# Kernel tuning notes

Measured on AMD Instinct MI355X. Metric: run time of the kernel, lower is better.

## Reference

```python
import jax, jax.numpy as jnp
import numpy as np

B, N, F, E, D, H, L = 4, 2048, 2, 16, 32, 4, 2
GRAPH_LAYERS = 3
FLOW_ITERS = 10
COST_C = 1.0        # quadratic cost: c*x^2, inv_derivative(y) = y/(2c)
BIG_NUMBER = 1e7


def setup_inputs():
    key = jax.random.key(0)
    ks = jax.random.split(key, 20)
    node_features = jax.random.normal(ks[0], (B, N, F), jnp.float32)
    node_embeddings = jax.random.normal(ks[1], (B, N, E), jnp.float32)
    demands = jax.random.normal(ks[2], (B, N, 1), jnp.float32)
    demands = demands - demands.mean(axis=1, keepdims=True)  # flow conservation
    adj = (jax.random.uniform(ks[3], (B, N, N)) < 0.01).astype(jnp.float32)
    adj = adj * (1.0 - jnp.eye(N, dtype=jnp.float32))
    eye = jnp.broadcast_to(jnp.eye(N, dtype=jnp.float32), (B, N, N))
    neighborhoods = jnp.stack([eye, adj], axis=1)  # [B,L,N,N] hop-0 and hop-1
    def g(k, shape):
        return jax.random.normal(k, shape, jnp.float32) * 0.1
    params = {
        'We1': g(ks[4], (E + F, D)), 'be1': jnp.zeros((D,), jnp.float32),
        'We2': g(ks[5], (D, D)), 'be2': jnp.zeros((D,), jnp.float32),
        'w_attn': g(ks[6], (H, D)),
        'Wo': g(ks[7], (D, D)), 'bo': jnp.zeros((D,), jnp.float32),
        'Wz': g(ks[8], (D, D)), 'Uz': g(ks[9], (D, D)), 'bz': jnp.zeros((D,), jnp.float32),
        'Wr': g(ks[10], (D, D)), 'Ur': g(ks[11], (D, D)), 'br': jnp.zeros((D,), jnp.float32),
        'Wh': g(ks[12], (D, D)), 'Uh': g(ks[13], (D, D)), 'bh': jnp.zeros((D,), jnp.float32),
        'Wd1': g(ks[14], (D, D)), 'bd1': jnp.zeros((D,), jnp.float32),
        'Wd2': g(ks[15], (D, 1)), 'bd2': jnp.zeros((1,), jnp.float32),
        'Wv1': g(ks[16], (D, D)), 'bv1': jnp.zeros((D,), jnp.float32),
        'Wv2': g(ks[17], (D, 1)), 'bv2': jnp.zeros((1,), jnp.float32),
    }
    return {'node_features': node_features, 'node_embeddings': node_embeddings,
            'demands': demands, 'adj': adj, 'neighborhoods': neighborhoods, **params}


def _forward(node_features, node_embeddings, demands, adj, neighborhoods,
             We1, be1, We2, be2, w_attn, Wo, bo,
             Wz, Uz, bz, Wr, Ur, br, Wh, Uh, bh,
             Wd1, bd1, Wd2, bd2, Wv1, bv1, Wv2, bv2):
    # --- node encoder MLP (tanh, activate_final=True) ---
    x = jnp.concatenate([node_embeddings, node_features], axis=-1)   # [B,N,E+F]
    enc = jnp.tanh(jnp.tanh(x @ We1 + be1) @ We2 + be2)               # [B,N,D]
    # row-normalized neighborhood operators (degree-normalized aggregation)
    Mnorm = neighborhoods / (jnp.sum(neighborhoods, axis=-1, keepdims=True) + 1.0)
    # --- graph_layers x (attention neighborhood + GRU state update) ---
    for _ in range(GRAPH_LAYERS):
        agg = jnp.einsum('blnm,bmd->blnd', Mnorm, enc)                # [B,L,N,D]
        scores = jnp.einsum('blnd,hd->bhnl', jnp.tanh(agg), w_attn)   # [B,H,N,L]
        alpha = jax.nn.softmax(scores, axis=-1)
        ctx = jnp.einsum('bhnl,blnd->bnd', alpha, agg) / H            # mean over heads
        nbr = jnp.tanh(ctx @ Wo + bo)                                 # [B,N,D]
        z = jax.nn.sigmoid(nbr @ Wz + enc @ Uz + bz)
        r = jax.nn.sigmoid(nbr @ Wr + enc @ Ur + br)
        h = jnp.tanh(nbr @ Wh + (r * enc) @ Uh + bh)
        enc = z * enc + (1.0 - z) * h
    # --- primal: edge weights, masked softmax, proportional flow solver ---
    pred = (enc @ Wd1 + bd1) @ Wd2 + bd2                              # [B,N,1]
    pw = pred * jnp.transpose(pred, (0, 2, 1))                        # [B,N,N]
    weights = -BIG_NUMBER * (1.0 - adj) + pw
    fwp = jax.nn.softmax(weights, axis=-1)                            # rows sum to 1
    flow0 = fwp * jax.nn.relu(-demands)

    def step(flow, _):
        inflow = jnp.sum(flow, axis=1)[..., None]                     # [B,N,1]
        return fwp * jax.nn.relu(inflow - demands), None

    flow, _ = jax.lax.scan(step, flow0, None, length=FLOW_ITERS)
    flow_cost = jnp.sum(COST_C * flow * flow, axis=(1, 2))            # [B]
    # --- dual: dual variables, dual flows via inverse cost derivative ---
    dual = (enc @ Wv1 + bv1) @ Wv2 + bv2                              # [B,N,1]
    dd = dual - jnp.transpose(dual, (0, 2, 1))                        # [B,N,N]
    df = adj * jax.nn.relu(dd / (2.0 * COST_C))
    dual_cost = jnp.sum(COST_C * df * df - dd * df, axis=(1, 2)) \
        - jnp.sum(dual * demands, axis=(1, 2))                        # [B]
    return flow_cost - dual_cost                                      # primal-dual gap loss, [B]


def reference(node_features, node_embeddings, demands, adj, neighborhoods,
              We1, be1, We2, be2, w_attn, Wo, bo,
              Wz, Uz, bz, Wr, Ur, br, Wh, Uh, bh,
              Wd1, bd1, Wd2, bd2, Wv1, bv1, Wv2, bv2):
    return _forward(node_features, node_embeddings, demands, adj, neighborhoods,
                    We1, be1, We2, be2, w_attn, Wo, bo,
                    Wz, Uz, bz, Wr, Ur, br, Wh, Uh, bh,
                    Wd1, bd1, Wd2, bd2, Wv1, bv1, Wv2, bv2)
```

## Files before the change

kernel.cpp:

```cpp
#include <hip/hip_runtime.h>

#define NN 2048
#define NB 4
#define BN (NB * NN)
#define MAXD 96

__global__ __launch_bounds__(256) void k_front(
    const float* __restrict__ feat, const float* __restrict__ emb,
    const float* __restrict__ We1, const float* __restrict__ be1,
    const float* __restrict__ We2, const float* __restrict__ be2,
    float* __restrict__ enc_out,
    const float* __restrict__ adj, int* __restrict__ deg, int* __restrict__ cols,
    int* __restrict__ tdeg)
{
    int tid = threadIdx.x;
    if (blockIdx.x < 1024) {
        __shared__ float sW1[18 * 32], sb1[32], sW2[32 * 32], sb2[32];
        for (int i = tid; i < 18 * 32; i += 256) sW1[i] = We1[i];
        for (int i = tid; i < 32 * 32; i += 256) sW2[i] = We2[i];
        if (tid < 32) { sb1[tid] = be1[tid]; sb2[tid] = be2[tid]; }
        __syncthreads();
        int group = tid >> 5, j = tid & 31;
        int node = blockIdx.x * 8 + group;
        float x;
        if (j < 16)      x = emb[node * 16 + j];
        else if (j < 18) x = feat[node * 2 + (j - 16)];
        else             x = 0.f;
        float acc = sb1[j];
#pragma unroll
        for (int k = 0; k < 18; k++)
            acc += __shfl(x, k, 32) * sW1[k * 32 + j];
        float h = tanhf(acc);
        float acc2 = sb2[j];
#pragma unroll
        for (int k = 0; k < 32; k++)
            acc2 += __shfl(h, k, 32) * sW2[k * 32 + j];
        enc_out[node * 32 + j] = tanhf(acc2);
    } else {
        int wave = tid >> 6, lane = tid & 63;
        int row = (blockIdx.x - 1024) * 4 + wave;
        const float4* p = (const float4*)(adj + (size_t)row * NN);
        int cnt = 0;
        int base = row * MAXD;
#pragma unroll
        for (int it = 0; it < 8; it++) {
            float4 v = p[it * 64 + lane];
            float va[4] = { v.x, v.y, v.z, v.w };
#pragma unroll
            for (int c = 0; c < 4; c++) {
                unsigned long long m = __ballot(va[c] != 0.f);
                if (va[c] != 0.f) {
                    int pos = cnt + __popcll(m & ((1ull << lane) - 1ull));
                    if (pos < MAXD) cols[base + pos] = it * 256 + lane * 4 + c;
                }
                cnt += __popcll(m);
            }
        }
        if (lane == 0) {
            deg[row] = cnt < MAXD ? cnt : MAXD;
            tdeg[row] = 0;
        }
    }
}

__global__ __launch_bounds__(256) void k_layer(
    const float* __restrict__ enc_in, float* __restrict__ enc_out,
    const int* __restrict__ deg, const int* __restrict__ cols,
    const float* __restrict__ w_attn,
    const float* __restrict__ Wo, const float* __restrict__ bo,
    const float* __restrict__ Wz, const float* __restrict__ Uz, const float* __restrict__ bz,
    const float* __restrict__ Wr, const float* __restrict__ Ur, const float* __restrict__ br,
    const float* __restrict__ Wh, const float* __restrict__ Uh, const float* __restrict__ bh)
{
    __shared__ float sWo[1024], sWz[1024], sUz[1024], sWr[1024], sUr[1024], sWh[1024], sUh[1024];
    __shared__ float sbo[32], sbz[32], sbr[32], sbh[32], sAttn[128];
    int tid = threadIdx.x;
    for (int i = tid; i < 1024; i += 256) {
        sWo[i] = Wo[i]; sWz[i] = Wz[i]; sUz[i] = Uz[i];
        sWr[i] = Wr[i]; sUr[i] = Ur[i]; sWh[i] = Wh[i]; sUh[i] = Uh[i];
    }
    if (tid < 32) { sbo[tid] = bo[tid]; sbz[tid] = bz[tid]; sbr[tid] = br[tid]; sbh[tid] = bh[tid]; }
    if (tid < 128) sAttn[tid] = w_attn[tid];
    __syncthreads();
    int group = tid >> 5, j = tid & 31;
    int node = blockIdx.x * 8 + group;
    int b = node >> 11;
    const float* encB = enc_in + (size_t)(b * NN) * 32;
    float e = enc_in[node * 32 + j];
    float agg0 = 0.5f * e;
    int d = deg[node];
    const int* cp = cols + node * MAXD;
    float a1 = 0.f;
    for (int i = 0; i < d; i++) {
        int m = cp[i];
        a1 += encB[m * 32 + j];
    }
    a1 *= 1.0f / (float)(d + 1);
    float t0 = tanhf(agg0), t1 = tanhf(a1);
    float sc[8];
#pragma unroll
    for (int h2 = 0; h2 < 4; h2++) { sc[h2] = sAttn[h2 * 32 + j] * t0; sc[4 + h2] = sAttn[h2 * 32 + j] * t1; }
#pragma unroll
    for (int off = 16; off >= 1; off >>= 1)
#pragma unroll
        for (int q = 0; q < 8; q++) sc[q] += __shfl_xor(sc[q], off, 32);
    float c0 = 0.f, c1 = 0.f;
#pragma unroll
    for (int h2 = 0; h2 < 4; h2++) {
        float a = sc[h2], bsc = sc[4 + h2];
        float mx = fmaxf(a, bsc);
        float e0 = expf(a - mx), e1 = expf(bsc - mx);
        float inv = 1.0f / (e0 + e1);
        c0 += e0 * inv; c1 += e1 * inv;
    }
    c0 *= 0.25f; c1 *= 0.25f;
    float ctx = c0 * agg0 + c1 * a1;
    float acc = sbo[j];
#pragma unroll
    for (int k = 0; k < 32; k++) acc += __shfl(ctx, k, 32) * sWo[k * 32 + j];
    float nbr = tanhf(acc);
    float az = sbz[j], ar = sbr[j], ah = sbh[j];
#pragma unroll
    for (int k = 0; k < 32; k++) {
        float nb = __shfl(nbr, k, 32);
        float en = __shfl(e, k, 32);
        az += nb * sWz[k * 32 + j] + en * sUz[k * 32 + j];
        ar += nb * sWr[k * 32 + j] + en * sUr[k * 32 + j];
        ah += nb * sWh[k * 32 + j];
    }
    float z = 1.0f / (1.0f + expf(-az));
    float r = 1.0f / (1.0f + expf(-ar));
    float re = r * e;
#pragma unroll
    for (int k = 0; k < 32; k++) ah += __shfl(re, k, 32) * sUh[k * 32 + j];
    float hc = tanhf(ah);
    enc_out[node * 32 + j] = z * e + (1.0f - z) * hc;
}

__global__ __launch_bounds__(256) void k_heads(
    const float* __restrict__ enc,
    const float* __restrict__ Wd1, const float* __restrict__ bd1,
    const float* __restrict__ Wd2, const float* __restrict__ bd2,
    const float* __restrict__ Wv1, const float* __restrict__ bv1,
    const float* __restrict__ Wv2, const float* __restrict__ bv2,
    float* __restrict__ pred, float* __restrict__ dual)
{
    __shared__ float sWd1[1024], sWv1[1024], sbd1[32], sbv1[32], sWd2[32], sWv2[32];
    int tid = threadIdx.x;
    for (int i = tid; i < 1024; i += 256) { sWd1[i] = Wd1[i]; sWv1[i] = Wv1[i]; }
    if (tid < 32) { sbd1[tid] = bd1[tid]; sbv1[tid] = bv1[tid]; sWd2[tid] = Wd2[tid]; sWv2[tid] = Wv2[tid]; }
    __syncthreads();
    int group = tid >> 5, j = tid & 31;
    int node = blockIdx.x * 8 + group;
    float e = enc[node * 32 + j];
    float ad = sbd1[j], av = sbv1[j];
#pragma unroll
    for (int k = 0; k < 32; k++) {
        float en = __shfl(e, k, 32);
        ad += en * sWd1[k * 32 + j];
        av += en * sWv1[k * 32 + j];
    }
    float pd = ad * sWd2[j];
    float dv = av * sWv2[j];
#pragma unroll
    for (int off = 16; off >= 1; off >>= 1) {
        pd += __shfl_xor(pd, off, 32);
        dv += __shfl_xor(dv, off, 32);
    }
    if (j == 0) {
        pred[node] = pd + bd2[0];
        dual[node] = dv + bv2[0];
    }
}

__global__ __launch_bounds__(256) void k_edge_scatter(
    const int* __restrict__ deg, const int* __restrict__ cols,
    const float* __restrict__ pred, const float* __restrict__ dual,
    int* __restrict__ tdeg, int* __restrict__ tcols, float* __restrict__ tvals,
    float* __restrict__ rowsq, float* __restrict__ rowdual)
{
    int wave = threadIdx.x >> 6, lane = threadIdx.x & 63;
    int row = blockIdx.x * 4 + wave;
    int b = row >> 11;
    int rloc = row & (NN - 1);
    const float* predB = pred + b * NN;
    const float* dualB = dual + b * NN;
    int d = deg[row];
    int base = row * MAXD;
    float pn = pred[row];
    float dn = dual[row];
    float mx = -1e30f;
    for (int i = lane; i < d; i += 64) {
        int c = cols[base + i];
        mx = fmaxf(mx, pn * predB[c]);
    }
#pragma unroll
    for (int off = 32; off >= 1; off >>= 1) mx = fmaxf(mx, __shfl_xor(mx, off));
    float den = 0.f, du = 0.f;
    for (int i = lane; i < d; i += 64) {
        int c = cols[base + i];
        den += expf(pn * predB[c] - mx);
        float dd = dn - dualB[c];
        if (dd > 0.f) du -= 0.25f * dd * dd;
    }
#pragma unroll
    for (int off = 32; off >= 1; off >>= 1) { den += __shfl_xor(den, off); du += __shfl_xor(du, off); }
    float invden = 1.0f / den;
    float rs = 0.f;
    for (int i = lane; i < d; i += 64) {
        int c = cols[base + i];
        float f = expf(pn * predB[c] - mx) * invden;
        rs += f * f;
        int pos = atomicAdd(&tdeg[b * NN + c], 1);
        if (pos < MAXD) {
            size_t idx = (size_t)(b * MAXD + pos) * NN + c;
            tcols[idx] = rloc;
            tvals[idx] = f;
        }
    }
#pragma unroll
    for (int off = 32; off >= 1; off >>= 1) rs += __shfl_xor(rs, off);
    if (lane == 0) { rowsq[row] = rs; rowdual[row] = du; }
}

__global__ __launch_bounds__(1024) void k_flow_batch(
    const int* __restrict__ tdeg, const int* __restrict__ tcols,
    const float* __restrict__ tvals, const float* __restrict__ demands,
    const float* __restrict__ rowsq, const float* __restrict__ rowdual,
    const float* __restrict__ dual, float* __restrict__ out)
{
    __shared__ float sdem[NN], sA[NN], sBuf[NN];
    __shared__ float red[3][16];
    int tid = threadIdx.x;
    int b = blockIdx.x;
    const float* demB = demands + b * NN;
    for (int n = tid; n < NN; n += 1024) {
        float dm = demB[n];
        sdem[n] = dm;
        sA[n] = fmaxf(-dm, 0.f);
    }
    __syncthreads();
    int n0 = tid, n1 = tid + 1024;
    int d0 = tdeg[b * NN + n0];
    int d1 = tdeg[b * NN + n1];
    const int* tc = tcols + (size_t)b * MAXD * NN;
    const float* tv = tvals + (size_t)b * MAXD * NN;
#pragma unroll 1
    for (int it = 0; it < 5; it++) {
        {
            float a0 = 0.f, a1 = 0.f;
            for (int i = 0; i < d0; i++) a0 += tv[i * NN + n0] * sA[tc[i * NN + n0]];
            for (int i = 0; i < d1; i++) a1 += tv[i * NN + n1] * sA[tc[i * NN + n1]];
            sBuf[n0] = fmaxf(a0 - sdem[n0], 0.f);
            sBuf[n1] = fmaxf(a1 - sdem[n1], 0.f);
        }
        __syncthreads();
        {
            float a0 = 0.f, a1 = 0.f;
            for (int i = 0; i < d0; i++) a0 += tv[i * NN + n0] * sBuf[tc[i * NN + n0]];
            for (int i = 0; i < d1; i++) a1 += tv[i * NN + n1] * sBuf[tc[i * NN + n1]];
            sA[n0] = fmaxf(a0 - sdem[n0], 0.f);
            sA[n1] = fmaxf(a1 - sdem[n1], 0.f);
        }
        __syncthreads();
    }
    float fc = 0.f, ds = 0.f, dq = 0.f;
    for (int n = tid; n < NN; n += 1024) {
        int row = b * NN + n;
        float sv = sA[n];
        fc += rowsq[row] * sv * sv;
        ds += rowdual[row];
        dq += dual[row] * sdem[n];
    }
#pragma unroll
    for (int off = 32; off >= 1; off >>= 1) {
        fc += __shfl_xor(fc, off);
        ds += __shfl_xor(ds, off);
        dq += __shfl_xor(dq, off);
    }
    int wv = tid >> 6;
    if ((tid & 63) == 0) { red[0][wv] = fc; red[1][wv] = ds; red[2][wv] = dq; }
    __syncthreads();
    if (tid == 0) {
        float a = 0.f, s1 = 0.f, s2 = 0.f;
        for (int w = 0; w < 16; w++) { a += red[0][w]; s1 += red[1][w]; s2 += red[2][w]; }
        out[b] = a - s1 + s2;
    }
}

extern "C" void kernel_launch(void* const* d_in, const int* in_sizes, int n_in,
                              void* d_out, int out_size, void* d_ws, size_t ws_size,
                              hipStream_t stream) {
    const float* feat = (const float*)d_in[0];
    const float* emb  = (const float*)d_in[1];
    const float* dem  = (const float*)d_in[2];
    const float* adj  = (const float*)d_in[3];
    const float* We1 = (const float*)d_in[5];
    const float* be1 = (const float*)d_in[6];
    const float* We2 = (const float*)d_in[7];
    const float* be2 = (const float*)d_in[8];
    const float* w_attn = (const float*)d_in[9];
    const float* Wo = (const float*)d_in[10];
    const float* bo = (const float*)d_in[11];
    const float* Wz = (const float*)d_in[12];
    const float* Uz = (const float*)d_in[13];
    const float* bz = (const float*)d_in[14];
    const float* Wr = (const float*)d_in[15];
    const float* Ur = (const float*)d_in[16];
    const float* br = (const float*)d_in[17];
    const float* Wh = (const float*)d_in[18];
    const float* Uh = (const float*)d_in[19];
    const float* bh = (const float*)d_in[20];
    const float* Wd1 = (const float*)d_in[21];
    const float* bd1 = (const float*)d_in[22];
    const float* Wd2 = (const float*)d_in[23];
    const float* bd2 = (const float*)d_in[24];
    const float* Wv1 = (const float*)d_in[25];
    const float* bv1 = (const float*)d_in[26];
    const float* Wv2 = (const float*)d_in[27];
    const float* bv2 = (const float*)d_in[28];
    float* out = (float*)d_out;

    float* w = (float*)d_ws;
    float* enc0 = w;            w += (size_t)BN * 32;
    float* enc1 = w;            w += (size_t)BN * 32;
    int*   degp = (int*)w;      w += BN;
    int*   colp = (int*)w;      w += (size_t)BN * MAXD;
    float* pred = w;            w += BN;
    float* dual = w;            w += BN;
    float* rowsq = w;           w += BN;
    float* rowdual = w;         w += BN;
    int*   tdeg = (int*)w;      w += BN;
    int*   tcol = (int*)w;      w += (size_t)BN * MAXD;
    float* tval = w;            w += (size_t)BN * MAXD;

    k_front<<<3072, 256, 0, stream>>>(feat, emb, We1, be1, We2, be2, enc0,
                                      adj, degp, colp, tdeg);
    k_layer<<<BN / 8, 256, 0, stream>>>(enc0, enc1, degp, colp, w_attn,
                                        Wo, bo, Wz, Uz, bz, Wr, Ur, br, Wh, Uh, bh);
    k_layer<<<BN / 8, 256, 0, stream>>>(enc1, enc0, degp, colp, w_attn,
                                        Wo, bo, Wz, Uz, bz, Wr, Ur, br, Wh, Uh, bh);
    k_layer<<<BN / 8, 256, 0, stream>>>(enc0, enc1, degp, colp, w_attn,
                                        Wo, bo, Wz, Uz, bz, Wr, Ur, br, Wh, Uh, bh);
    k_heads<<<BN / 8, 256, 0, stream>>>(enc1, Wd1, bd1, Wd2, bd2, Wv1, bv1, Wv2, bv2,
                                        pred, dual);
    k_edge_scatter<<<BN / 4, 256, 0, stream>>>(degp, colp, pred, dual,
                                               tdeg, tcol, tval, rowsq, rowdual);
    k_flow_batch<<<NB, 1024, 0, stream>>>(tdeg, tcol, tval, dem,
                                          rowsq, rowdual, dual, out);
}
```

Before: 461.5 us.

## Pack transposed edges per node as float2 and shuffle-broadcast neighbor indices

The transposed edge storage changes from separate column-major index and value arrays to a per-node contiguous array of (value, column) float2 pairs, which the flow kernel reads as float4 with two accumulators. The layer kernel loads neighbor indices once per lane and broadcasts them via warp shuffles, with dual accumulators. The aim is to cut index-load latency and serial dependency chains. The packed per-node layout makes adjacent threads read strided addresses, so it gives up the coalescing of the previous layout.

```diff
diff --git a/kernel.cpp b/kernel.cpp
--- a/kernel.cpp
+++ b/kernel.cpp
@@ -90,12 +90,24 @@
     float agg0 = 0.5f * e;
     int d = deg[node];
     const int* cp = cols + node * MAXD;
-    float a1 = 0.f;
-    for (int i = 0; i < d; i++) {
-        int m = cp[i];
+    int iA = cp[j];
+    int iB = cp[j + 32];
+    float a1 = 0.f, a1b = 0.f;
+    int dmin = d < 32 ? d : 32;
+#pragma unroll 4
+    for (int i = 0; i < dmin - 1; i += 2) {
+        int m0 = __shfl(iA, i, 32);
+        int m1 = __shfl(iA, i + 1, 32);
+        a1  += encB[m0 * 32 + j];
+        a1b += encB[m1 * 32 + j];
+    }
+    if (dmin & 1) { int m = __shfl(iA, dmin - 1, 32); a1 += encB[m * 32 + j]; }
+#pragma unroll 2
+    for (int i = 32; i < d; i++) {
+        int m = __shfl(iB, i - 32, 32);
         a1 += encB[m * 32 + j];
     }
-    a1 *= 1.0f / (float)(d + 1);
+    a1 = (a1 + a1b) * (1.0f / (float)(d + 1));
     float t0 = tanhf(agg0), t1 = tanhf(a1);
     float sc[8];
 #pragma unroll
@@ -176,7 +188,7 @@
 __global__ __launch_bounds__(256) void k_edge_scatter(
     const int* __restrict__ deg, const int* __restrict__ cols,
     const float* __restrict__ pred, const float* __restrict__ dual,
-    int* __restrict__ tdeg, int* __restrict__ tcols, float* __restrict__ tvals,
+    int* __restrict__ tdeg, float2* __restrict__ pk,
     float* __restrict__ rowsq, float* __restrict__ rowdual)
 {
     int wave = threadIdx.x >> 6, lane = threadIdx.x & 63;
@@ -213,9 +225,7 @@
         rs += f * f;
         int pos = atomicAdd(&tdeg[b * NN + c], 1);
         if (pos < MAXD) {
-            size_t idx = (size_t)(b * MAXD + pos) * NN + c;
-            tcols[idx] = rloc;
-            tvals[idx] = f;
+            pk[((size_t)(b * NN) + c) * MAXD + pos] = make_float2(f, __int_as_float(rloc));
         }
     }
 #pragma unroll
@@ -223,9 +233,31 @@
     if (lane == 0) { rowsq[row] = rs; rowdual[row] = du; }
 }
 
+#define FLOW_GATHER(EPTR, PAIRS, REM, DTOT, SRC, ACC_A, ACC_B)                     \
+    {                                                                              \
+        int i_ = 0;                                                                \
+        for (; i_ + 1 < (PAIRS); i_ += 2) {                                        \
+            float4 qa_ = (EPTR)[i_];                                               \
+            float4 qb_ = (EPTR)[i_ + 1];                                           \
+            ACC_A += qa_.x * SRC[__float_as_int(qa_.y)];                           \
+            ACC_B += qa_.z * SRC[__float_as_int(qa_.w)];                           \
+            ACC_A += qb_.x * SRC[__float_as_int(qb_.y)];                           \
+            ACC_B += qb_.z * SRC[__float_as_int(qb_.w)];                           \
+        }                                                                          \
+        if (i_ < (PAIRS)) {                                                        \
+            float4 q_ = (EPTR)[i_];                                                \
+            ACC_A += q_.x * SRC[__float_as_int(q_.y)];                             \
+            ACC_B += q_.z * SRC[__float_as_int(q_.w)];                             \
+        }                                                                          \
+        if (REM) {                                                                 \
+            float2 q_ = ((const float2*)(EPTR))[(DTOT) - 1];                       \
+            ACC_A += q_.x * SRC[__float_as_int(q_.y)];                             \
+        }                                                                          \
+    }
+
 __global__ __launch_bounds__(1024) void k_flow_batch(
-    const int* __restrict__ tdeg, const int* __restrict__ tcols,
-    const float* __restrict__ tvals, const float* __restrict__ demands,
+    const int* __restrict__ tdeg, const float2* __restrict__ pk,
+    const float* __restrict__ demands,
     const float* __restrict__ rowsq, const float* __restrict__ rowdual,
     const float* __restrict__ dual, float* __restrict__ out)
 {
@@ -243,24 +275,27 @@
     int n0 = tid, n1 = tid + 1024;
     int d0 = tdeg[b * NN + n0];
     int d1 = tdeg[b * NN + n1];
-    const int* tc = tcols + (size_t)b * MAXD * NN;
-    const float* tv = tvals + (size_t)b * MAXD * NN;
+    const float4* e0 = (const float4*)(pk + ((size_t)(b * NN) + n0) * MAXD);
+    const float4* e1 = (const float4*)(pk + ((size_t)(b * NN) + n1) * MAXD);
+    int p0 = d0 >> 1, r0 = d0 & 1;
+    int p1 = d1 >> 1, r1 = d1 & 1;
+    float dm0 = sdem[n0], dm1 = sdem[n1];
 #pragma unroll 1
     for (int it = 0; it < 5; it++) {
         {
-            float a0 = 0.f, a1 = 0.f;
-            for (int i = 0; i < d0; i++) a0 += tv[i * NN + n0] * sA[tc[i * NN + n0]];
-            for (int i = 0; i < d1; i++) a1 += tv[i * NN + n1] * sA[tc[i * NN + n1]];
-            sBuf[n0] = fmaxf(a0 - sdem[n0], 0.f);
-            sBuf[n1] = fmaxf(a1 - sdem[n1], 0.f);
+            float a0 = 0.f, a0b = 0.f, a1 = 0.f, a1b = 0.f;
+            FLOW_GATHER(e0, p0, r0, d0, sA, a0, a0b);
+            FLOW_GATHER(e1, p1, r1, d1, sA, a1, a1b);
+            sBuf[n0] = fmaxf(a0 + a0b - dm0, 0.f);
+            sBuf[n1] = fmaxf(a1 + a1b - dm1, 0.f);
         }
         __syncthreads();
         {
-            float a0 = 0.f, a1 = 0.f;
-            for (int i = 0; i < d0; i++) a0 += tv[i * NN + n0] * sBuf[tc[i * NN + n0]];
-            for (int i = 0; i < d1; i++) a1 += tv[i * NN + n1] * sBuf[tc[i * NN + n1]];
-            sA[n0] = fmaxf(a0 - sdem[n0], 0.f);
-            sA[n1] = fmaxf(a1 - sdem[n1], 0.f);
+            float a0 = 0.f, a0b = 0.f, a1 = 0.f, a1b = 0.f;
+            FLOW_GATHER(e0, p0, r0, d0, sBuf, a0, a0b);
+            FLOW_GATHER(e1, p1, r1, d1, sBuf, a1, a1b);
+            sA[n0] = fmaxf(a0 + a0b - dm0, 0.f);
+            sA[n1] = fmaxf(a1 + a1b - dm1, 0.f);
         }
         __syncthreads();
     }
@@ -331,8 +366,7 @@
     float* rowsq = w;           w += BN;
     float* rowdual = w;         w += BN;
     int*   tdeg = (int*)w;      w += BN;
-    int*   tcol = (int*)w;      w += (size_t)BN * MAXD;
-    float* tval = w;            w += (size_t)BN * MAXD;
+    float2* pk = (float2*)w;    w += (size_t)BN * MAXD * 2;
 
     k_front<<<3072, 256, 0, stream>>>(feat, emb, We1, be1, We2, be2, enc0,
                                       adj, degp, colp, tdeg);
@@ -345,7 +379,7 @@
     k_heads<<<BN / 8, 256, 0, stream>>>(enc1, Wd1, bd1, Wd2, bd2, Wv1, bv1, Wv2, bv2,
                                         pred, dual);
     k_edge_scatter<<<BN / 4, 256, 0, stream>>>(degp, colp, pred, dual,
-                                               tdeg, tcol, tval, rowsq, rowdual);
-    k_flow_batch<<<NB, 1024, 0, stream>>>(tdeg, tcol, tval, dem,
+                                               tdeg, pk, rowsq, rowdual);
+    k_flow_batch<<<NB, 1024, 0, stream>>>(tdeg, pk, dem,
                                           rowsq, rowdual, dual, out);
 }
```

Measured after the change: 476.3 us. 1.03x slower.

## Fuse heads into last GNN layer, enlarge layer blocks, shuffle-broadcast neighbor indices

Applied to the files above, without the earlier changes.

The last graph layer now also computes the decoder and dual heads, which removes one kernel launch and the round trip of the final encoding through global memory. Layer blocks grow from 256 to 1024 threads (32 nodes per block), so the shared-memory weight staging is spread over more nodes. Neighbor indices are loaded once per lane and broadcast with shuffles, and the gather loop uses two accumulators to overlap loads. The larger blocks raise per-block shared memory and may limit occupancy, and the dual accumulators change floating-point summation order.

```diff
diff --git a/kernel.cpp b/kernel.cpp
--- a/kernel.cpp
+++ b/kernel.cpp
@@ -63,7 +63,75 @@
     }
 }
 
-__global__ __launch_bounds__(256) void k_layer(
+__device__ __forceinline__ float layer_body(
+    int node, int j, int d, const int* __restrict__ cp,
+    const float* __restrict__ encB, float e,
+    const float* sAttn, const float* sWo, const float* sbo,
+    const float* sWz, const float* sUz, const float* sbz,
+    const float* sWr, const float* sUr, const float* sbr,
+    const float* sWh, const float* sUh, const float* sbh)
+{
+    float agg0 = 0.5f * e;
+    int iA = cp[j];
+    int iB = cp[j + 32];
+    float a1 = 0.f, a1b = 0.f;
+    int dmin = d < 32 ? d : 32;
+#pragma unroll 4
+    for (int i = 0; i < dmin - 1; i += 2) {
+        int m0 = __shfl(iA, i, 32);
+        int m1 = __shfl(iA, i + 1, 32);
+        a1  += encB[m0 * 32 + j];
+        a1b += encB[m1 * 32 + j];
+    }
+    if (dmin & 1) { int m = __shfl(iA, dmin - 1, 32); a1 += encB[m * 32 + j]; }
+#pragma unroll 2
+    for (int i = 32; i < d; i++) {
+        int m = __shfl(iB, i - 32, 32);
+        a1 += encB[m * 32 + j];
+    }
+    a1 = (a1 + a1b) * (1.0f / (float)(d + 1));
+    float t0 = tanhf(agg0), t1 = tanhf(a1);
+    float sc[8];
+#pragma unroll
+    for (int h2 = 0; h2 < 4; h2++) { sc[h2] = sAttn[h2 * 32 + j] * t0; sc[4 + h2] = sAttn[h2 * 32 + j] * t1; }
+#pragma unroll
+    for (int off = 16; off >= 1; off >>= 1)
+#pragma unroll
+        for (int q = 0; q < 8; q++) sc[q] += __shfl_xor(sc[q], off, 32);
+    float c0 = 0.f, c1 = 0.f;
+#pragma unroll
+    for (int h2 = 0; h2 < 4; h2++) {
+        float a = sc[h2], bsc = sc[4 + h2];
+        float mx = fmaxf(a, bsc);
+        float e0 = expf(a - mx), e1 = expf(bsc - mx);
+        float inv = 1.0f / (e0 + e1);
+        c0 += e0 * inv; c1 += e1 * inv;
+    }
+    c0 *= 0.25f; c1 *= 0.25f;
+    float ctx = c0 * agg0 + c1 * a1;
+    float acc = sbo[j];
+#pragma unroll
+    for (int k = 0; k < 32; k++) acc += __shfl(ctx, k, 32) * sWo[k * 32 + j];
+    float nbr = tanhf(acc);
+    float az = sbz[j], ar = sbr[j], ah = sbh[j];
+#pragma unroll
+    for (int k = 0; k < 32; k++) {
+        float nb = __shfl(nbr, k, 32);
+        float en = __shfl(e, k, 32);
+        az += nb * sWz[k * 32 + j] + en * sUz[k * 32 + j];
+        ar += nb * sWr[k * 32 + j] + en * sUr[k * 32 + j];
+        ah += nb * sWh[k * 32 + j];
+    }
+    float z = 1.0f / (1.0f + expf(-az));
+    float r = 1.0f / (1.0f + expf(-ar));
+    float re = r * e;
+#pragma unroll
+    for (int k = 0; k < 32; k++) ah += __shfl(re, k, 32) * sUh[k * 32 + j];
+    float hc = tanhf(ah);
+    return z * e + (1.0f - z) * hc;
+}
+
+__global__ __launch_bounds__(1024) void k_layer(
     const float* __restrict__ enc_in, float* __restrict__ enc_out,
     const int* __restrict__ deg, const int* __restrict__ cols,
     const float* __restrict__ w_attn,
@@ -75,7 +143,8 @@
     __shared__ float sWo[1024], sWz[1024], sUz[1024], sWr[1024], sUr[1024], sWh[1024], sUh[1024];
     __shared__ float sbo[32], sbz[32], sbr[32], sbh[32], sAttn[128];
     int tid = threadIdx.x;
-    for (int i = tid; i < 1024; i += 256) {
+    {
+        int i = tid;
         sWo[i] = Wo[i]; sWz[i] = Wz[i]; sUz[i] = Uz[i];
         sWr[i] = Wr[i]; sUr[i] = Ur[i]; sWh[i] = Wh[i]; sUh[i] = Uh[i];
     }
@@ -83,80 +152,61 @@
     if (tid < 128) sAttn[tid] = w_attn[tid];
     __syncthreads();
     int group = tid >> 5, j = tid & 31;
-    int node = blockIdx.x * 8 + group;
+    int node = blockIdx.x * 32 + group;
     int b = node >> 11;
     const float* encB = enc_in + (size_t)(b * NN) * 32;
     float e = enc_in[node * 32 + j];
-    float agg0 = 0.5f * e;
     int d = deg[node];
     const int* cp = cols + node * MAXD;
-    float a1 = 0.f;
-    for (int i = 0; i < d; i++) {
-        int m = cp[i];
-        a1 += encB[m * 32 + j];
-    }
-    a1 *= 1.0f / (float)(d + 1);
-    float t0 = tanhf(agg0), t1 = tanhf(a1);
-    float sc[8];
-#pragma unroll
-    for (int h2 = 0; h2 < 4; h2++) { sc[h2] = sAttn[h2 * 32 + j] * t0; sc[4 + h2] = sAttn[h2 * 32 + j] * t1; }
-#pragma unroll
-    for (int off = 16; off >= 1; off >>= 1)
-#pragma unroll
-        for (int q = 0; q < 8; q++) sc[q] += __shfl_xor(sc[q], off, 32);
-    float c0 = 0.f, c1 = 0.f;
-#pragma unroll
-    for (int h2 = 0; h2 < 4; h2++) {
-        float a = sc[h2], bsc = sc[4 + h2];
-        float mx = fmaxf(a, bsc);
-        float e0 = expf(a - mx), e1 = expf(bsc - mx);
-        float inv = 1.0f / (e0 + e1);
-        c0 += e0 * inv; c1 += e1 * inv;
-    }
-    c0 *= 0.25f; c1 *= 0.25f;
-    float ctx = c0 * agg0 + c1 * a1;
-    float acc = sbo[j];
-#pragma unroll
-    for (int k = 0; k < 32; k++) acc += __shfl(ctx, k, 32) * sWo[k * 32 + j];
-    float nbr = tanhf(acc);
-    float az = sbz[j], ar = sbr[j], ah = sbh[j];
-#pragma unroll
-    for (int k = 0; k < 32; k++) {
-        float nb = __shfl(nbr, k, 32);
-        float en = __shfl(e, k, 32);
-        az += nb * sWz[k * 32 + j] + en * sUz[k * 32 + j];
-        ar += nb * sWr[k * 32 + j] + en * sUr[k * 32 + j];
-        ah += nb * sWh[k * 32 + j];
-    }
-    float z = 1.0f / (1.0f + expf(-az));
-    float r = 1.0f / (1.0f + expf(-ar));
-    float re = r * e;
-#pragma unroll
-    for (int k = 0; k < 32; k++) ah += __shfl(re, k, 32) * sUh[k * 32 + j];
-    float hc = tanhf(ah);
-    enc_out[node * 32 + j] = z * e + (1.0f - z) * hc;
-}
-
-__global__ __launch_bounds__(256) void k_heads(
-    const float* __restrict__ enc,
+    float eo = layer_body(node, j, d, cp, encB, e, sAttn, sWo, sbo,
+                          sWz, sUz, sbz, sWr, sUr, sbr, sWh, sUh, sbh);
+    enc_out[node * 32 + j] = eo;
+}
+
+__global__ __launch_bounds__(1024) void k_layer_last(
+    const float* __restrict__ enc_in,
+    const int* __restrict__ deg, const int* __restrict__ cols,
+    const float* __restrict__ w_attn,
+    const float* __restrict__ Wo, const float* __restrict__ bo,
+    const float* __restrict__ Wz, const float* __restrict__ Uz, const float* __restrict__ bz,
+    const float* __restrict__ Wr, const float* __restrict__ Ur, const float* __restrict__ br,
+    const float* __restrict__ Wh, const float* __restrict__ Uh, const float* __restrict__ bh,
     const float* __restrict__ Wd1, const float* __restrict__ bd1,
     const float* __restrict__ Wd2, const float* __restrict__ bd2,
     const float* __restrict__ Wv1, const float* __restrict__ bv1,
     const float* __restrict__ Wv2, const float* __restrict__ bv2,
     float* __restrict__ pred, float* __restrict__ dual)
 {
-    __shared__ float sWd1[1024], sWv1[1024], sbd1[32], sbv1[32], sWd2[32], sWv2[32];
+    __shared__ float sWo[1024], sWz[1024], sUz[1024], sWr[1024], sUr[1024], sWh[1024], sUh[1024];
+    __shared__ float sWd1[1024], sWv1[1024];
+    __shared__ float sbo[32], sbz[32], sbr[32], sbh[32], sAttn[128];
+    __shared__ float sbd1[32], sbv1[32], sWd2[32], sWv2[32];
     int tid = threadIdx.x;
-    for (int i = tid; i < 1024; i += 256) { sWd1[i] = Wd1[i]; sWv1[i] = Wv1[i]; }
-    if (tid < 32) { sbd1[tid] = bd1[tid]; sbv1[tid] = bv1[tid]; sWd2[tid] = Wd2[tid]; sWv2[tid] = Wv2[tid]; }
+    {
+        int i = tid;
+        sWo[i] = Wo[i]; sWz[i] = Wz[i]; sUz[i] = Uz[i];
+        sWr[i] = Wr[i]; sUr[i] = Ur[i]; sWh[i] = Wh[i]; sUh[i] = Uh[i];
+        sWd1[i] = Wd1[i]; sWv1[i] = Wv1[i];
+    }
+    if (tid < 32) {
+        sbo[tid] = bo[tid]; sbz[tid] = bz[tid]; sbr[tid] = br[tid]; sbh[tid] = bh[tid];
+        sbd1[tid] = bd1[tid]; sbv1[tid] = bv1[tid]; sWd2[tid] = Wd2[tid]; sWv2[tid] = Wv2[tid];
+    }
+    if (tid < 128) sAttn[tid] = w_attn[tid];
     __syncthreads();
     int group = tid >> 5, j = tid & 31;
-    int node = blockIdx.x * 8 + group;
-    float e = enc[node * 32 + j];
+    int node = blockIdx.x * 32 + group;
+    int b = node >> 11;
+    const float* encB = enc_in + (size_t)(b * NN) * 32;
+    float e = enc_in[node * 32 + j];
+    int d = deg[node];
+    const int* cp = cols + node * MAXD;
+    float eo = layer_body(node, j, d, cp, encB, e, sAttn, sWo, sbo,
+                          sWz, sUz, sbz, sWr, sUr, sbr, sWh, sUh, sbh);
     float ad = sbd1[j], av = sbv1[j];
 #pragma unroll
     for (int k = 0; k < 32; k++) {
-        float en = __shfl(e, k, 32);
+        float en = __shfl(eo, k, 32);
         ad += en * sWd1[k * 32 + j];
         av += en * sWv1[k * 32 + j];
     }
@@ -336,14 +386,14 @@
 
     k_front<<<3072, 256, 0, stream>>>(feat, emb, We1, be1, We2, be2, enc0,
                                       adj, degp, colp, tdeg);
-    k_layer<<<BN / 8, 256, 0, stream>>>(enc0, enc1, degp, colp, w_attn,
-                                        Wo, bo, Wz, Uz, bz, Wr, Ur, br, Wh, Uh, bh);
-    k_layer<<<BN / 8, 256, 0, stream>>>(enc1, enc0, degp, colp, w_attn,
-                                        Wo, bo, Wz, Uz, bz, Wr, Ur, br, Wh, Uh, bh);
-    k_layer<<<BN / 8, 256, 0, stream>>>(enc0, enc1, degp, colp, w_attn,
-                                        Wo, bo, Wz, Uz, bz, Wr, Ur, br, Wh, Uh, bh);
-    k_heads<<<BN / 8, 256, 0, stream>>>(enc1, Wd1, bd1, Wd2, bd2, Wv1, bv1, Wv2, bv2,
-                                        pred, dual);
+    k_layer<<<BN / 32, 1024, 0, stream>>>(enc0, enc1, degp, colp, w_attn,
+                                          Wo, bo, Wz, Uz, bz, Wr, Ur, br, Wh, Uh, bh);
+    k_layer<<<BN / 32, 1024, 0, stream>>>(enc1, enc0, degp, colp, w_attn,
+                                          Wo, bo, Wz, Uz, bz, Wr, Ur, br, Wh, Uh, bh);
+    k_layer_last<<<BN / 32, 1024, 0, stream>>>(enc0, degp, colp, w_attn,
+                                               Wo, bo, Wz, Uz, bz, Wr, Ur, br, Wh, Uh, bh,
+                                               Wd1, bd1, Wd2, bd2, Wv1, bv1, Wv2, bv2,
+                                               pred, dual);
     k_edge_scatter<<<BN / 4, 256, 0, stream>>>(degp, colp, pred, dual,
                                                tdeg, tcol, tval, rowsq, rowdual);
     k_flow_batch<<<NB, 1024, 0, stream>>>(tdeg, tcol, tval, dem,
```

Result: faster. 424.5 us (-8.0%).
